# Kernel tuning notes

Hardware: AMD Instinct MI355X
Metric: run time of the kernel (lower is better)

The kernel has to match this reference:

```python
import jax, jax.numpy as jnp
import numpy as np

C = 64            # x_channel (d_model)
D = 2 * C         # d_inner (expand=2)
N = C // 2        # d_state
K = 4             # scan directions
R = -(-C // 16)   # dt_rank = ceil(d_model/16)
Bsz, H, W = 2, 48, 48
EPS = 1e-5


def setup_inputs() -> dict:
    key = jax.random.key(0)
    ks = jax.random.split(key, 8)
    g = lambda k, shp, s: jax.random.normal(k, shp, dtype=jnp.float32) * s
    return {
        "fufea1": g(ks[0], (Bsz, C, H, W), 1.0),
        "ln_g": jnp.ones((C,), jnp.float32),
        "ln_b": jnp.zeros((C,), jnp.float32),
        "in_proj_w": g(ks[1], (2 * D, C), C ** -0.5),
        "conv_w": g(ks[2], (D, 1, 3, 3), 1.0 / 3.0),   # depthwise 3x3
        "conv_b": g(ks[3], (D,), 0.02),
        "x_proj_w": g(ks[4], (K, R + 2 * N, D), D ** -0.5),
        "dt_w": g(ks[5], (K, D, R), R ** -0.5),
        "dt_b": g(ks[6], (K, D), 0.1),
        "A_logs": jnp.log(jnp.tile(jnp.arange(1, N + 1, dtype=jnp.float32), (K, D, 1))),  # S4D-real init
        "Ds": jnp.ones((K, D), jnp.float32),
        "out_ln_g": jnp.ones((D,), jnp.float32),
        "out_ln_b": jnp.zeros((D,), jnp.float32),
        "out_proj_w": g(ks[7], (C, D), D ** -0.5),
    }


def _layernorm(x, g, b):
    mu = x.mean(-1, keepdims=True)
    var = ((x - mu) ** 2).mean(-1, keepdims=True)
    return (x - mu) * jax.lax.rsqrt(var + EPS) * g + b


def reference(fufea1, ln_g, ln_b, in_proj_w, conv_w, conv_b, x_proj_w,
              dt_w, dt_b, A_logs, Ds, out_ln_g, out_ln_b, out_proj_w):
    B, Cc, Hh, Ww = fufea1.shape
    L = Hh * Ww
    # pre-LN (over channels, channels-last)
    xn = _layernorm(fufea1.transpose(0, 2, 3, 1), ln_g, ln_b)          # (B,H,W,C)
    # SS2D: in_proj -> split x,z
    xz = xn @ in_proj_w.T                                               # (B,H,W,2D)
    x, z = jnp.split(xz, 2, axis=-1)
    x = x.transpose(0, 3, 1, 2)                                         # (B,D,H,W)
    x = jax.lax.conv_general_dilated(x, conv_w, (1, 1), "SAME",
                                     feature_group_count=D,
                                     dimension_numbers=("NCHW", "OIHW", "NCHW"))
    x = jax.nn.silu(x + conv_b[None, :, None, None])
    # 4-direction sequences: row-major, col-major, and their reverses
    x_hw = x.reshape(B, D, L)
    x_wh = x.transpose(0, 1, 3, 2).reshape(B, D, L)
    xs = jnp.stack([x_hw, x_wh], axis=1)                                # (B,2,D,L)
    xs = jnp.concatenate([xs, jnp.flip(xs, axis=-1)], axis=1)           # (B,K,D,L)
    # per-direction projections of dt, B, C
    x_dbl = jnp.einsum("bkdl,kcd->bkcl", xs, x_proj_w)
    dts, Bs, Cs = jnp.split(x_dbl, [R, R + N], axis=2)                  # (B,K,R,L),(B,K,N,L),(B,K,N,L)
    dts = jnp.einsum("bkrl,kdr->bkdl", dts, dt_w)
    delta = jax.nn.softplus(dts + dt_b[None, :, :, None])               # (B,K,D,L)
    A = -jnp.exp(A_logs)                                                # (K,D,N)
    # selective scan over L; carry h: (B,K,D,N)
    u_l = xs.transpose(3, 0, 1, 2)                                      # (L,B,K,D)
    dt_l = delta.transpose(3, 0, 1, 2)
    B_l = Bs.transpose(3, 0, 1, 2)                                      # (L,B,K,N)
    C_l = Cs.transpose(3, 0, 1, 2)

    def step(h, inp):
        u_t, d_t, b_t, c_t = inp
        dA = jnp.exp(d_t[..., None] * A)                                # (B,K,D,N)
        h = dA * h + (d_t * u_t)[..., None] * b_t[:, :, None, :]
        y = jnp.einsum("bkdn,bkn->bkd", h, c_t)
        return h, y

    h0 = jnp.zeros((B, K, D, N), xs.dtype)
    _, ys = jax.lax.scan(step, h0, (u_l, dt_l, B_l, C_l))               # ys: (L,B,K,D)
    out_y = ys.transpose(1, 2, 3, 0) + Ds[None, :, :, None] * xs        # (B,K,D,L)
    # merge the 4 directions back to row-major hw order
    inv_y = jnp.flip(out_y[:, 2:4], axis=-1)                            # (B,2,D,L)
    wh = lambda t: t.reshape(B, D, Ww, Hh).transpose(0, 1, 3, 2).reshape(B, D, L)
    y = out_y[:, 0] + inv_y[:, 0] + wh(out_y[:, 1]) + wh(inv_y[:, 1])   # (B,D,L)
    y = y.transpose(0, 2, 1).reshape(B, Hh, Ww, D)
    y = _layernorm(y, out_ln_g, out_ln_b) * jax.nn.silu(z)
    out = (y @ out_proj_w.T).transpose(0, 3, 1, 2) + fufea1             # residual add
    return out
```

## Files before the change

### kernel.cpp

```cpp
#include <hip/hip_runtime.h>

#define Cc 64
#define Dd 128
#define Nn 32
#define Kk 4
#define Rr 4
#define Bb 2
#define Hh 48
#define Ww 48
#define Ll 2304
#define EPSf 1e-5f
#define LCc 144

#if __has_builtin(__builtin_amdgcn_exp2f)
#define EXP2F __builtin_amdgcn_exp2f
#else
#define EXP2F exp2f
#endif

__device__ __forceinline__ float wsum64(float v) {
  v += __shfl_xor(v, 32);
  v += __shfl_xor(v, 16);
  v += __shfl_xor(v, 8);
  v += __shfl_xor(v, 4);
  v += __shfl_xor(v, 2);
  v += __shfl_xor(v, 1);
  return v;
}

__global__ __launch_bounds__(256) void k1_ln_inproj(
    const float* __restrict__ x, const float* __restrict__ g,
    const float* __restrict__ bta, const float* __restrict__ Wp,
    float* __restrict__ xin, float* __restrict__ zb)
{
  __shared__ float xS[16][65];
  __shared__ float xnS[16][64];
  __shared__ float xaS[128][17];
  const int tid = threadIdx.x;
  const int wv = tid >> 6, lane = tid & 63;
  const int pbase = blockIdx.x * 16;
  const int b = pbase / Ll;
  const int lbase = pbase % Ll;
  {
    const int c = tid >> 2, li0 = (tid & 3) * 4;
    const float4 v4 = *(const float4*)&x[(b * Cc + c) * Ll + lbase + li0];
    xS[li0 + 0][c] = v4.x;
    xS[li0 + 1][c] = v4.y;
    xS[li0 + 2][c] = v4.z;
    xS[li0 + 3][c] = v4.w;
  }
  __syncthreads();
  const float gv = g[lane], bv = bta[lane];
  for (int pi = 0; pi < 4; ++pi) {
    const int p = wv * 4 + pi;
    const float v = xS[p][lane];
    const float mu = wsum64(v) * (1.0f / 64.0f);
    const float dv = v - mu;
    const float var = wsum64(dv * dv) * (1.0f / 64.0f);
    const float rs = rsqrtf(var + EPSf);
    xnS[p][lane] = dv * rs * gv + bv;
  }
  __syncthreads();
  float acc[4][4];
  #pragma unroll
  for (int pi = 0; pi < 4; ++pi)
    #pragma unroll
    for (int m = 0; m < 4; ++m) acc[pi][m] = 0.f;
  const float4* W4 = (const float4*)Wp;
  #pragma unroll 4
  for (int c4 = 0; c4 < 16; ++c4) {
    float4 xn4[4];
    #pragma unroll
    for (int pi = 0; pi < 4; ++pi)
      xn4[pi] = ((const float4*)xnS[wv * 4 + pi])[c4];
    #pragma unroll
    for (int m = 0; m < 4; ++m) {
      const float4 w4 = W4[(lane + 64 * m) * 16 + c4];
      #pragma unroll
      for (int pi = 0; pi < 4; ++pi)
        acc[pi][m] += xn4[pi].x * w4.x + xn4[pi].y * w4.y +
                      xn4[pi].z * w4.z + xn4[pi].w * w4.w;
    }
  }
  #pragma unroll
  for (int pi = 0; pi < 4; ++pi) {
    const int l = lbase + wv * 4 + pi;
    zb[(b * Ll + l) * Dd + lane]      = acc[pi][2];
    zb[(b * Ll + l) * Dd + lane + 64] = acc[pi][3];
    xaS[lane][wv * 4 + pi]      = acc[pi][0];
    xaS[lane + 64][wv * 4 + pi] = acc[pi][1];
  }
  __syncthreads();
  const int d = tid >> 1, off = (tid & 1) * 8;
  float* dst = &xin[(b * Dd + d) * Ll + lbase + off];
  #pragma unroll
  for (int i = 0; i < 8; ++i) dst[i] = xaS[d][off + i];
}

__global__ __launch_bounds__(512) void k3_proj(
    const float* __restrict__ xin, const float* __restrict__ cw,
    const float* __restrict__ cb, const float* __restrict__ xpw,
    const float* __restrict__ dtw, const float* __restrict__ dtb,
    float* __restrict__ xc, float2* __restrict__ dd2,
    float* __restrict__ Bm, float* __restrict__ Cm)
{
  __shared__ float xinS[128][30];
  __shared__ float xvS[8][132];
  __shared__ float dtsS[8][16];
  const int t = threadIdx.x;
  const int pb = blockIdx.x * 8;
  const int b = pb / Ll;
  const int lb = pb % Ll;
  const int h0 = lb / Ww, w0 = lb % Ww;
  for (int i = t; i < 3840; i += 512) {
    const int d = i / 30, j = i % 30;
    const int r = j / 10, c = j % 10;
    const int hh = h0 + r - 1, ww = w0 + c - 1;
    float v = 0.f;
    if (hh >= 0 && hh < Hh && ww >= 0 && ww < Ww)
      v = xin[(b * Dd + d) * Ll + hh * Ww + ww];
    xinS[d][j] = v;
  }
  __syncthreads();
  for (int i = t; i < 1024; i += 512) {
    const int pi = i >> 7, d = i & 127;
    float acc = cb[d];
    #pragma unroll
    for (int r = 0; r < 3; ++r)
      #pragma unroll
      for (int c = 0; c < 3; ++c)
        acc += xinS[d][r * 10 + pi + c] * cw[d * 9 + r * 3 + c];
    const float sig = 1.0f / (1.0f + __expf(-acc));
    xvS[pi][d] = acc * sig;
  }
  __syncthreads();
  for (int i = t; i < 1024; i += 512) {
    const int d = i >> 3, pi = i & 7;
    xc[(b * Dd + d) * Ll + lb + pi] = xvS[pi][d];
  }
  if (t < 272) {
    const int k = t / 68, c = t % 68;
    const size_t bkL = (size_t)(b * Kk + k) * Ll;
    float acc[8];
    #pragma unroll
    for (int pi = 0; pi < 8; ++pi) acc[pi] = 0.f;
    const float4* w4p = (const float4*)(xpw + (k * 68 + c) * 128);
    for (int d4 = 0; d4 < 32; ++d4) {
      const float4 w4 = w4p[d4];
      #pragma unroll
      for (int pi = 0; pi < 8; ++pi) {
        const float4 x4 = ((const float4*)xvS[pi])[d4];
        acc[pi] += x4.x * w4.x + x4.y * w4.y + x4.z * w4.z + x4.w * w4.w;
      }
    }
    #pragma unroll
    for (int pi = 0; pi < 8; ++pi) {
      const int l0 = lb + pi;
      const int h = l0 / Ww, w = l0 % Ww;
      int lk;
      if      (k == 0) lk = l0;
      else if (k == 1) lk = w * Hh + h;
      else if (k == 2) lk = Ll - 1 - l0;
      else             lk = Ll - 1 - (w * Hh + h);
      if (c < Rr)            dtsS[pi][k * 4 + c] = acc[pi];
      else if (c < Rr + Nn)  Bm[(bkL + lk) * Nn + (c - Rr)] = acc[pi];
      else                   Cm[(bkL + lk) * Nn + (c - Rr - Nn)] = acc[pi];
    }
  }
  __syncthreads();
  {
    const int k = t >> 7, dd = t & 127;
    const float4 dw = *(const float4*)&dtw[(k * Dd + dd) * 4];
    const float biasv = dtb[k * Dd + dd];
    float2* drow = dd2 + ((size_t)((b * Kk + k) * Dd) + dd) * Ll;
    float2 buf[8];
    #pragma unroll
    for (int pi = 0; pi < 8; ++pi) {
      const float a = biasv
          + dtsS[pi][k * 4 + 0] * dw.x + dtsS[pi][k * 4 + 1] * dw.y
          + dtsS[pi][k * 4 + 2] * dw.z + dtsS[pi][k * 4 + 3] * dw.w;
      const float sp = (a > 20.f) ? a : log1pf(__expf(a));
      buf[pi] = make_float2(sp, sp * xvS[pi][dd]);
    }
    if (k == 0) {
      float4* f4 = (float4*)(drow + lb);
      #pragma unroll
      for (int j = 0; j < 4; ++j)
        f4[j] = make_float4(buf[2 * j].x, buf[2 * j].y, buf[2 * j + 1].x, buf[2 * j + 1].y);
    } else if (k == 2) {
      float4* f4 = (float4*)(drow + (Ll - 8 - lb));
      #pragma unroll
      for (int j = 0; j < 4; ++j)
        f4[j] = make_float4(buf[7 - 2 * j].x, buf[7 - 2 * j].y, buf[6 - 2 * j].x, buf[6 - 2 * j].y);
    } else {
      #pragma unroll
      for (int pi = 0; pi < 8; ++pi) {
        const int l0 = lb + pi;
        const int h = l0 / Ww, w = l0 % Ww;
        int lk = w * Hh + h;
        if (k == 3) lk = Ll - 1 - lk;
        drow[lk] = buf[pi];
      }
    }
  }
}

__global__ __launch_bounds__(512) void k4_scan(
    const float2* __restrict__ dd2, const float* __restrict__ Bm,
    const float* __restrict__ Cm, const float* __restrict__ Alogs,
    float* __restrict__ ys)
{
  __shared__ float hendS[16][32];
  __shared__ float carryS[16][32];
  __shared__ float sumDS[16];
  __shared__ float pS[16][8][36];
  const int tid = threadIdx.x;
  const int s = tid >> 5, n = tid & 31;
  const int blk = blockIdx.x;
  const int bk = blk & 7;
  const int d = blk >> 3;
  const int b = bk >> 2, k = bk & 3;
  const float An = -__expf(Alogs[(k * Dd + d) * Nn + n]);
  const float AnE = An * 1.44269504f;
  const size_t bkL = (size_t)(b * Kk + k) * Ll;
  const float2* dP = dd2 + ((size_t)((b * Kk + k) * Dd) + d) * Ll;
  const float* bP = Bm + bkL * Nn + n;
  const float* cP = Cm + bkL * Nn + n;
  const int lbeg = s * LCc;
  float hA = 0.f, sumD = 0.f;
  {
    const float4* q4 = (const float4*)(dP + lbeg);
    const float* bl = bP + (size_t)lbeg * Nn;
    float4 qa = q4[0], qb = q4[1];
    float b0 = bl[0], b1 = bl[Nn], b2 = bl[2 * Nn], b3 = bl[3 * Nn];
    for (int it = 0; it < LCc / 4; ++it) {
      q4 += 2; bl += 4 * Nn;
      const float4 qa_n = q4[0], qb_n = q4[1];
      const float b0n = bl[0], b1n = bl[Nn], b2n = bl[2 * Nn], b3n = bl[3 * Nn];
      hA = EXP2F(qa.x * AnE) * hA + qa.y * b0;
      hA = EXP2F(qa.z * AnE) * hA + qa.w * b1;
      hA = EXP2F(qb.x * AnE) * hA + qb.y * b2;
      hA = EXP2F(qb.z * AnE) * hA + qb.w * b3;
      sumD += (qa.x + qa.z) + (qb.x + qb.z);
      qa = qa_n; qb = qb_n; b0 = b0n; b1 = b1n; b2 = b2n; b3 = b3n;
    }
  }
  hendS[s][n] = hA;
  if (n == 0) sumDS[s] = sumD;
  __syncthreads();
  if (tid < 32) {
    float carry = 0.f;
    #pragma unroll
    for (int s2 = 0; s2 < 16; ++s2) {
      carryS[s2][tid] = carry;
      carry = EXP2F(AnE * sumDS[s2]) * carry + hendS[s2][tid];
    }
  }
  __syncthreads();
  float h = carryS[s][n];
  float* yP = ys + ((size_t)((b * Kk + k) * Dd) + d) * Ll + lbeg;
  const float4* q4 = (const float4*)(dP + lbeg);
  const float* bl = bP + (size_t)lbeg * Nn;
  const float* cl = cP + (size_t)lbeg * Nn;
  const int rrow = n & 7, qtr = n >> 3;
  float4 qa = q4[0], qb = q4[1];
  float b0 = bl[0], b1 = bl[Nn], b2 = bl[2 * Nn], b3 = bl[3 * Nn];
  float c0 = cl[0], c1 = cl[Nn], c2 = cl[2 * Nn], c3 = cl[3 * Nn];
  for (int t8 = 0; t8 < LCc / 8; ++t8) {
    #pragma unroll
    for (int half = 0; half < 2; ++half) {
      q4 += 2; bl += 4 * Nn; cl += 4 * Nn;
      const float4 qa_n = q4[0], qb_n = q4[1];
      const float b0n = bl[0], b1n = bl[Nn], b2n = bl[2 * Nn], b3n = bl[3 * Nn];
      const float c0n = cl[0], c1n = cl[Nn], c2n = cl[2 * Nn], c3n = cl[3 * Nn];
      h = EXP2F(qa.x * AnE) * h + qa.y * b0; pS[s][half * 4 + 0][n] = h * c0;
      h = EXP2F(qa.z * AnE) * h + qa.w * b1; pS[s][half * 4 + 1][n] = h * c1;
      h = EXP2F(qb.x * AnE) * h + qb.y * b2; pS[s][half * 4 + 2][n] = h * c2;
      h = EXP2F(qb.z * AnE) * h + qb.w * b3; pS[s][half * 4 + 3][n] = h * c3;
      qa = qa_n; qb = qb_n; b0 = b0n; b1 = b1n; b2 = b2n; b3 = b3n;
      c0 = c0n; c1 = c1n; c2 = c2n; c3 = c3n;
    }
    const float4 a4 = *(const float4*)&pS[s][rrow][qtr * 8];
    const float4 d4 = *(const float4*)&pS[s][rrow][qtr * 8 + 4];
    float sum = ((a4.x + a4.y) + (a4.z + a4.w)) + ((d4.x + d4.y) + (d4.z + d4.w));
    sum += __shfl_xor(sum, 8);
    sum += __shfl_xor(sum, 16);
    if (n < 8) yP[t8 * 8 + n] = sum;
  }
}

__global__ __launch_bounds__(256) void k5_merge(
    const float* __restrict__ ys, const float* __restrict__ zb,
    const float* __restrict__ og, const float* __restrict__ ob,
    const float* __restrict__ Wo, const float* __restrict__ resid,
    const float* __restrict__ xc, const float* __restrict__ DsP,
    float* __restrict__ out)
{
  __shared__ float ysS[4][16][128];
  __shared__ float tS[16][128];
  __shared__ float oS[64][17];
  __shared__ float xcS[16][128];
  const int tid = threadIdx.x;
  const int wv = tid >> 6, lane = tid & 63;
  const int pbase = blockIdx.x * 16;
  const int b = pbase / Ll;
  const int lbase = pbase % Ll;
  const int hrow = lbase / Ww, w0 = lbase % Ww;
  {
    const int dch = tid & 127, seg = tid >> 7;
    {
      const float4 a4 = *(const float4*)&xc[(b * Dd + dch) * Ll + lbase + seg * 8];
      const float4 c4 = *(const float4*)&xc[(b * Dd + dch) * Ll + lbase + seg * 8 + 4];
      xcS[seg * 8 + 0][dch] = a4.x; xcS[seg * 8 + 1][dch] = a4.y;
      xcS[seg * 8 + 2][dch] = a4.z; xcS[seg * 8 + 3][dch] = a4.w;
      xcS[seg * 8 + 4][dch] = c4.x; xcS[seg * 8 + 5][dch] = c4.y;
      xcS[seg * 8 + 6][dch] = c4.z; xcS[seg * 8 + 7][dch] = c4.w;
    }
    {
      const size_t r0 = ((size_t)(b * Kk + 0) * Dd + dch) * Ll + lbase + seg * 8;
      const float4 a4 = *(const float4*)&ys[r0];
      const float4 c4 = *(const float4*)&ys[r0 + 4];
      ysS[0][seg * 8 + 0][dch] = a4.x; ysS[0][seg * 8 + 1][dch] = a4.y;
      ysS[0][seg * 8 + 2][dch] = a4.z; ysS[0][seg * 8 + 3][dch] = a4.w;
      ysS[0][seg * 8 + 4][dch] = c4.x; ysS[0][seg * 8 + 5][dch] = c4.y;
      ysS[0][seg * 8 + 6][dch] = c4.z; ysS[0][seg * 8 + 7][dch] = c4.w;
    }
    {
      const size_t r2 = ((size_t)(b * Kk + 2) * Dd + dch) * Ll + (Ll - 16 - lbase) + seg * 8;
      const float4 a4 = *(const float4*)&ys[r2];
      const float4 c4 = *(const float4*)&ys[r2 + 4];
      ysS[2][15 - seg * 8 - 0][dch] = a4.x; ysS[2][15 - seg * 8 - 1][dch] = a4.y;
      ysS[2][15 - seg * 8 - 2][dch] = a4.z; ysS[2][15 - seg * 8 - 3][dch] = a4.w;
      ysS[2][15 - seg * 8 - 4][dch] = c4.x; ysS[2][15 - seg * 8 - 5][dch] = c4.y;
      ysS[2][15 - seg * 8 - 6][dch] = c4.z; ysS[2][15 - seg * 8 - 7][dch] = c4.w;
    }
    {
      const size_t r1 = ((size_t)(b * Kk + 1) * Dd + dch) * Ll;
      const size_t r3 = ((size_t)(b * Kk + 3) * Dd + dch) * Ll;
      #pragma unroll
      for (int j = 0; j < 8; ++j) {
        const int p = seg * 8 + j;
        const int l1 = (w0 + p) * Hh + hrow;
        ysS[1][p][dch] = ys[r1 + l1];
        ysS[3][p][dch] = ys[r3 + (Ll - 1 - l1)];
      }
    }
  }
  float sDs[2];
  #pragma unroll
  for (int m = 0; m < 2; ++m) {
    const int dch = lane + 64 * m;
    sDs[m] = DsP[dch] + DsP[Dd + dch] + DsP[2 * Dd + dch] + DsP[3 * Dd + dch];
  }
  __syncthreads();
  for (int pi = 0; pi < 4; ++pi) {
    const int p = wv * 4 + pi;
    const int l0 = lbase + p;
    float tv[2];
    #pragma unroll
    for (int m = 0; m < 2; ++m) {
      const int dch = lane + 64 * m;
      tv[m] = ysS[0][p][dch] + ysS[1][p][dch] + ysS[2][p][dch] + ysS[3][p][dch]
            + sDs[m] * xcS[p][dch];
    }
    const float mu = wsum64(tv[0] + tv[1]) * (1.0f / 128.0f);
    const float q = wsum64((tv[0] - mu) * (tv[0] - mu) +
                           (tv[1] - mu) * (tv[1] - mu)) * (1.0f / 128.0f);
    const float rs = rsqrtf(q + EPSf);
    #pragma unroll
    for (int m = 0; m < 2; ++m) {
      const int dch = lane + 64 * m;
      const float zz = zb[(size_t)(b * Ll + l0) * Dd + dch];
      const float sig = 1.0f / (1.0f + __expf(-zz));
      tS[p][dch] = ((tv[m] - mu) * rs * og[dch] + ob[dch]) * (zz * sig);
    }
  }
  __syncthreads();
  float acc[4] = {0.f, 0.f, 0.f, 0.f};
  const float4* W4 = (const float4*)Wo;
  for (int d4 = 0; d4 < 32; ++d4) {
    const float4 w4 = W4[lane * 32 + d4];
    #pragma unroll
    for (int pi = 0; pi < 4; ++pi) {
      const float4 t4 = ((const float4*)tS[wv * 4 + pi])[d4];
      acc[pi] += t4.x * w4.x + t4.y * w4.y + t4.z * w4.z + t4.w * w4.w;
    }
  }
  #pragma unroll
  for (int pi = 0; pi < 4; ++pi) oS[lane][wv * 4 + pi] = acc[pi];
  __syncthreads();
  const int c = tid >> 2, off = (tid & 3) * 4;
  const size_t obase = (size_t)(b * Cc + c) * Ll + lbase + off;
  const float4 r4 = *(const float4*)(resid + obase);
  float4 o4;
  o4.x = oS[c][off + 0] + r4.x;
  o4.y = oS[c][off + 1] + r4.y;
  o4.z = oS[c][off + 2] + r4.z;
  o4.w = oS[c][off + 3] + r4.w;
  *(float4*)(out + obase) = o4;
}

extern "C" void kernel_launch(void* const* d_in, const int* in_sizes, int n_in,
                              void* d_out, int out_size, void* d_ws, size_t ws_size,
                              hipStream_t stream)
{
  (void)in_sizes; (void)n_in; (void)out_size; (void)ws_size;
  const float* fufea1     = (const float*)d_in[0];
  const float* ln_g       = (const float*)d_in[1];
  const float* ln_b       = (const float*)d_in[2];
  const float* in_proj_w  = (const float*)d_in[3];
  const float* conv_w     = (const float*)d_in[4];
  const float* conv_b     = (const float*)d_in[5];
  const float* x_proj_w   = (const float*)d_in[6];
  const float* dt_w       = (const float*)d_in[7];
  const float* dt_b       = (const float*)d_in[8];
  const float* A_logs     = (const float*)d_in[9];
  const float* Ds         = (const float*)d_in[10];
  const float* out_ln_g   = (const float*)d_in[11];
  const float* out_ln_b   = (const float*)d_in[12];
  const float* out_proj_w = (const float*)d_in[13];

  float* ws = (float*)d_ws;
  float2* dd2 = (float2*)ws;
  float* Bm   = ws + 4718592;
  float* Cm   = ws + 5308416;
  float* zb   = ws + 5898240;
  float* xc   = ws + 6488064;
  float* ysb  = ws + 7077888;
  float* xin  = ws + 7077888;

  k1_ln_inproj<<<288, 256, 0, stream>>>(fufea1, ln_g, ln_b, in_proj_w, xin, zb);
  k3_proj<<<576, 512, 0, stream>>>(xin, conv_w, conv_b, x_proj_w, dt_w, dt_b,
                                   xc, dd2, Bm, Cm);
  k4_scan<<<1024, 512, 0, stream>>>(dd2, Bm, Cm, A_logs, ysb);
  k5_merge<<<288, 256, 0, stream>>>(ysb, zb, out_ln_g, out_ln_b, out_proj_w, fufea1,
                                    xc, Ds, (float*)d_out);
}
```

Baseline: 218.3 us.

## Single-pass chunked scan with truncated carry correction and transposed B/C layout

The chunked selective scan now runs once, starting each chunk from a zero state and writing outputs directly, instead of a separate state pass followed by a full recompute pass. After the carry between chunks is computed, only the decaying carry contribution is added back, and that loop stops early once the decay makes it negligible according to a bound built from the carry size, the largest |C| and the slowest decay rate. B and C are also stored with time as the innermost dimension so each lane can read them as float4 vectors. This removes roughly half of the scan arithmetic and memory traffic. In exchange the result is approximate, with error controlled by a fixed threshold, and the correction adds a serial shuffle reduction per timestep.

New measurement: 378.5 us. 73.4% more time.

```diff
diff --git a/kernel.cpp b/kernel.cpp
--- a/kernel.cpp
+++ b/kernel.cpp
@@ -25,6 +25,15 @@
   v += __shfl_xor(v, 4);
   v += __shfl_xor(v, 2);
   v += __shfl_xor(v, 1);
+  return v;
+}
+
+__device__ __forceinline__ float hmax32(float v) {
+  v = fmaxf(v, __shfl_xor(v, 1));
+  v = fmaxf(v, __shfl_xor(v, 2));
+  v = fmaxf(v, __shfl_xor(v, 4));
+  v = fmaxf(v, __shfl_xor(v, 8));
+  v = fmaxf(v, __shfl_xor(v, 16));
   return v;
 }
 
@@ -140,7 +149,6 @@
   }
   if (t < 272) {
     const int k = t / 68, c = t % 68;
-    const size_t bkL = (size_t)(b * Kk + k) * Ll;
     float acc[8];
     #pragma unroll
     for (int pi = 0; pi < 8; ++pi) acc[pi] = 0.f;
@@ -162,9 +170,12 @@
       else if (k == 1) lk = w * Hh + h;
       else if (k == 2) lk = Ll - 1 - l0;
       else             lk = Ll - 1 - (w * Hh + h);
-      if (c < Rr)            dtsS[pi][k * 4 + c] = acc[pi];
-      else if (c < Rr + Nn)  Bm[(bkL + lk) * Nn + (c - Rr)] = acc[pi];
-      else                   Cm[(bkL + lk) * Nn + (c - Rr - Nn)] = acc[pi];
+      if (c < Rr)
+        dtsS[pi][k * 4 + c] = acc[pi];
+      else if (c < Rr + Nn)
+        Bm[((size_t)(b * Kk + k) * Nn + (c - Rr)) * Ll + lk] = acc[pi];
+      else
+        Cm[((size_t)(b * Kk + k) * Nn + (c - Rr - Nn)) * Ll + lk] = acc[pi];
     }
   }
   __syncthreads();
@@ -213,6 +224,7 @@
   __shared__ float hendS[16][32];
   __shared__ float carryS[16][32];
   __shared__ float sumDS[16];
+  __shared__ float cmaxS[16];
   __shared__ float pS[16][8][36];
   const int tid = threadIdx.x;
   const int s = tid >> 5, n = tid & 31;
@@ -222,31 +234,45 @@
   const int b = bk >> 2, k = bk & 3;
   const float An = -__expf(Alogs[(k * Dd + d) * Nn + n]);
   const float AnE = An * 1.44269504f;
-  const size_t bkL = (size_t)(b * Kk + k) * Ll;
   const float2* dP = dd2 + ((size_t)((b * Kk + k) * Dd) + d) * Ll;
-  const float* bP = Bm + bkL * Nn + n;
-  const float* cP = Cm + bkL * Nn + n;
+  const size_t rowBC = (size_t)(b * Kk + k) * Nn + n;
+  const float* bRow = Bm + rowBC * Ll;
+  const float* cRow = Cm + rowBC * Ll;
   const int lbeg = s * LCc;
-  float hA = 0.f, sumD = 0.f;
-  {
-    const float4* q4 = (const float4*)(dP + lbeg);
-    const float* bl = bP + (size_t)lbeg * Nn;
-    float4 qa = q4[0], qb = q4[1];
-    float b0 = bl[0], b1 = bl[Nn], b2 = bl[2 * Nn], b3 = bl[3 * Nn];
-    for (int it = 0; it < LCc / 4; ++it) {
-      q4 += 2; bl += 4 * Nn;
+  float* yP = ys + ((size_t)((b * Kk + k) * Dd) + d) * Ll + lbeg;
+
+  float h = 0.f, sumD = 0.f, cmx = 0.f;
+  const float4* q4 = (const float4*)(dP + lbeg);
+  const float4* b4 = (const float4*)(bRow + lbeg);
+  const float4* c4 = (const float4*)(cRow + lbeg);
+  const int rrow = n & 7, qtr = n >> 3;
+  float4 qa = q4[0], qb = q4[1];
+  float4 bv = b4[0], cv = c4[0];
+  for (int t8 = 0; t8 < LCc / 8; ++t8) {
+    #pragma unroll
+    for (int half = 0; half < 2; ++half) {
+      q4 += 2; b4 += 1; c4 += 1;
       const float4 qa_n = q4[0], qb_n = q4[1];
-      const float b0n = bl[0], b1n = bl[Nn], b2n = bl[2 * Nn], b3n = bl[3 * Nn];
-      hA = EXP2F(qa.x * AnE) * hA + qa.y * b0;
-      hA = EXP2F(qa.z * AnE) * hA + qa.w * b1;
-      hA = EXP2F(qb.x * AnE) * hA + qb.y * b2;
-      hA = EXP2F(qb.z * AnE) * hA + qb.w * b3;
+      const float4 bv_n = b4[0], cv_n = c4[0];
+      h = EXP2F(qa.x * AnE) * h + qa.y * bv.x; pS[s][half * 4 + 0][n] = h * cv.x;
+      h = EXP2F(qa.z * AnE) * h + qa.w * bv.y; pS[s][half * 4 + 1][n] = h * cv.y;
+      h = EXP2F(qb.x * AnE) * h + qb.y * bv.z; pS[s][half * 4 + 2][n] = h * cv.z;
+      h = EXP2F(qb.z * AnE) * h + qb.w * bv.w; pS[s][half * 4 + 3][n] = h * cv.w;
       sumD += (qa.x + qa.z) + (qb.x + qb.z);
-      qa = qa_n; qb = qb_n; b0 = b0n; b1 = b1n; b2 = b2n; b3 = b3n;
-    }
-  }
-  hendS[s][n] = hA;
-  if (n == 0) sumDS[s] = sumD;
+      cmx = fmaxf(cmx, fmaxf(fmaxf(fabsf(cv.x), fabsf(cv.y)),
+                             fmaxf(fabsf(cv.z), fabsf(cv.w))));
+      qa = qa_n; qb = qb_n; bv = bv_n; cv = cv_n;
+    }
+    const float4 a4 = *(const float4*)&pS[s][rrow][qtr * 8];
+    const float4 d4v = *(const float4*)&pS[s][rrow][qtr * 8 + 4];
+    float sum = ((a4.x + a4.y) + (a4.z + a4.w)) + ((d4v.x + d4v.y) + (d4v.z + d4v.w));
+    sum += __shfl_xor(sum, 8);
+    sum += __shfl_xor(sum, 16);
+    if (n < 8) yP[t8 * 8 + n] = sum;
+  }
+  hendS[s][n] = h;
+  const float cmxAll = hmax32(cmx);
+  if (n == 0) { sumDS[s] = sumD; cmaxS[s] = cmxAll; }
   __syncthreads();
   if (tid < 32) {
     float carry = 0.f;
@@ -257,35 +283,27 @@
     }
   }
   __syncthreads();
-  float h = carryS[s][n];
-  float* yP = ys + ((size_t)((b * Kk + k) * Dd) + d) * Ll + lbeg;
-  const float4* q4 = (const float4*)(dP + lbeg);
-  const float* bl = bP + (size_t)lbeg * Nn;
-  const float* cl = cP + (size_t)lbeg * Nn;
-  const int rrow = n & 7, qtr = n >> 3;
-  float4 qa = q4[0], qb = q4[1];
-  float b0 = bl[0], b1 = bl[Nn], b2 = bl[2 * Nn], b3 = bl[3 * Nn];
-  float c0 = cl[0], c1 = cl[Nn], c2 = cl[2 * Nn], c3 = cl[3 * Nn];
-  for (int t8 = 0; t8 < LCc / 8; ++t8) {
-    #pragma unroll
-    for (int half = 0; half < 2; ++half) {
-      q4 += 2; bl += 4 * Nn; cl += 4 * Nn;
-      const float4 qa_n = q4[0], qb_n = q4[1];
-      const float b0n = bl[0], b1n = bl[Nn], b2n = bl[2 * Nn], b3n = bl[3 * Nn];
-      const float c0n = cl[0], c1n = cl[Nn], c2n = cl[2 * Nn], c3n = cl[3 * Nn];
-      h = EXP2F(qa.x * AnE) * h + qa.y * b0; pS[s][half * 4 + 0][n] = h * c0;
-      h = EXP2F(qa.z * AnE) * h + qa.w * b1; pS[s][half * 4 + 1][n] = h * c1;
-      h = EXP2F(qb.x * AnE) * h + qb.y * b2; pS[s][half * 4 + 2][n] = h * c2;
-      h = EXP2F(qb.z * AnE) * h + qb.w * b3; pS[s][half * 4 + 3][n] = h * c3;
-      qa = qa_n; qb = qb_n; b0 = b0n; b1 = b1n; b2 = b2n; b3 = b3n;
-      c0 = c0n; c1 = c1n; c2 = c2n; c3 = c3n;
-    }
-    const float4 a4 = *(const float4*)&pS[s][rrow][qtr * 8];
-    const float4 d4 = *(const float4*)&pS[s][rrow][qtr * 8 + 4];
-    float sum = ((a4.x + a4.y) + (a4.z + a4.w)) + ((d4.x + d4.y) + (d4.z + d4.w));
-    sum += __shfl_xor(sum, 8);
-    sum += __shfl_xor(sum, 16);
-    if (n < 8) yP[t8 * 8 + n] = sum;
+  const float carry = carryS[s][n];
+  const float mc = hmax32(fabsf(carry));
+  const float AmaxE = hmax32(AnE);
+  const float Pstop = log2f(mc * cmaxS[s] * 3.2e6f) / (-AmaxE);
+  if (Pstop > 0.f) {
+    float hc = carry, P = 0.f;
+    const float2* dQ = dP + lbeg;
+    const float* cQ = cRow + lbeg;
+    for (int t = 0; t < LCc; ++t) {
+      if (P >= Pstop) break;
+      const float dlt = dQ[t].x;
+      hc *= EXP2F(dlt * AnE);
+      P += dlt;
+      float contrib = hc * cQ[t];
+      contrib += __shfl_xor(contrib, 1);
+      contrib += __shfl_xor(contrib, 2);
+      contrib += __shfl_xor(contrib, 4);
+      contrib += __shfl_xor(contrib, 8);
+      contrib += __shfl_xor(contrib, 16);
+      if (n == 0) yP[t] += contrib;
+    }
   }
 }
 
```

## Split chunked scan into local pass plus early-terminating carry correction

Applied to the files above, without the earlier changes.

The first pass of the chunked selective scan now runs from a zero state and writes each chunk's local outputs directly. The second pass no longer re-runs the full recurrence. It propagates only the incoming carry, which is decayed by the cumulative dt times A, and adds its contribution to y. That pass stops once a bound built from the running max of |C|, the max |carry| and the slowest-decaying A shows the remaining contribution is negligible. This removes most of the second read of dt, B and C, at the cost of a read-modify-write of y and a tolerance-based truncation that adds small absolute error.

Measured after the change: 202.6 us. 1.08x faster.

```diff
diff --git a/kernel.cpp b/kernel.cpp
--- a/kernel.cpp
+++ b/kernel.cpp
@@ -25,6 +25,15 @@
   v += __shfl_xor(v, 4);
   v += __shfl_xor(v, 2);
   v += __shfl_xor(v, 1);
+  return v;
+}
+
+__device__ __forceinline__ float hmax32(float v) {
+  v = fmaxf(v, __shfl_xor(v, 1));
+  v = fmaxf(v, __shfl_xor(v, 2));
+  v = fmaxf(v, __shfl_xor(v, 4));
+  v = fmaxf(v, __shfl_xor(v, 8));
+  v = fmaxf(v, __shfl_xor(v, 16));
   return v;
 }
 
@@ -213,6 +222,7 @@
   __shared__ float hendS[16][32];
   __shared__ float carryS[16][32];
   __shared__ float sumDS[16];
+  __shared__ float cmaxS[16];
   __shared__ float pS[16][8][36];
   const int tid = threadIdx.x;
   const int s = tid >> 5, n = tid & 31;
@@ -227,26 +237,45 @@
   const float* bP = Bm + bkL * Nn + n;
   const float* cP = Cm + bkL * Nn + n;
   const int lbeg = s * LCc;
-  float hA = 0.f, sumD = 0.f;
+  float* yP = ys + ((size_t)((b * Kk + k) * Dd) + d) * Ll + lbeg;
+  const int rrow = n & 7, qtr = n >> 3;
+
+  float h = 0.f, sumD = 0.f, cmx = 0.f;
   {
     const float4* q4 = (const float4*)(dP + lbeg);
     const float* bl = bP + (size_t)lbeg * Nn;
+    const float* cl = cP + (size_t)lbeg * Nn;
     float4 qa = q4[0], qb = q4[1];
     float b0 = bl[0], b1 = bl[Nn], b2 = bl[2 * Nn], b3 = bl[3 * Nn];
-    for (int it = 0; it < LCc / 4; ++it) {
-      q4 += 2; bl += 4 * Nn;
-      const float4 qa_n = q4[0], qb_n = q4[1];
-      const float b0n = bl[0], b1n = bl[Nn], b2n = bl[2 * Nn], b3n = bl[3 * Nn];
-      hA = EXP2F(qa.x * AnE) * hA + qa.y * b0;
-      hA = EXP2F(qa.z * AnE) * hA + qa.w * b1;
-      hA = EXP2F(qb.x * AnE) * hA + qb.y * b2;
-      hA = EXP2F(qb.z * AnE) * hA + qb.w * b3;
-      sumD += (qa.x + qa.z) + (qb.x + qb.z);
-      qa = qa_n; qb = qb_n; b0 = b0n; b1 = b1n; b2 = b2n; b3 = b3n;
-    }
-  }
-  hendS[s][n] = hA;
-  if (n == 0) sumDS[s] = sumD;
+    float c0 = cl[0], c1 = cl[Nn], c2 = cl[2 * Nn], c3 = cl[3 * Nn];
+    for (int t8 = 0; t8 < LCc / 8; ++t8) {
+      #pragma unroll
+      for (int half = 0; half < 2; ++half) {
+        q4 += 2; bl += 4 * Nn; cl += 4 * Nn;
+        const float4 qa_n = q4[0], qb_n = q4[1];
+        const float b0n = bl[0], b1n = bl[Nn], b2n = bl[2 * Nn], b3n = bl[3 * Nn];
+        const float c0n = cl[0], c1n = cl[Nn], c2n = cl[2 * Nn], c3n = cl[3 * Nn];
+        h = EXP2F(qa.x * AnE) * h + qa.y * b0; pS[s][half * 4 + 0][n] = h * c0;
+        h = EXP2F(qa.z * AnE) * h + qa.w * b1; pS[s][half * 4 + 1][n] = h * c1;
+        h = EXP2F(qb.x * AnE) * h + qb.y * b2; pS[s][half * 4 + 2][n] = h * c2;
+        h = EXP2F(qb.z * AnE) * h + qb.w * b3; pS[s][half * 4 + 3][n] = h * c3;
+        sumD += (qa.x + qa.z) + (qb.x + qb.z);
+        cmx = fmaxf(cmx, fmaxf(fmaxf(fabsf(c0), fabsf(c1)),
+                               fmaxf(fabsf(c2), fabsf(c3))));
+        qa = qa_n; qb = qb_n; b0 = b0n; b1 = b1n; b2 = b2n; b3 = b3n;
+        c0 = c0n; c1 = c1n; c2 = c2n; c3 = c3n;
+      }
+      const float4 a4 = *(const float4*)&pS[s][rrow][qtr * 8];
+      const float4 d4v = *(const float4*)&pS[s][rrow][qtr * 8 + 4];
+      float sum = ((a4.x + a4.y) + (a4.z + a4.w)) + ((d4v.x + d4v.y) + (d4v.z + d4v.w));
+      sum += __shfl_xor(sum, 8);
+      sum += __shfl_xor(sum, 16);
+      if (n < 8) yP[t8 * 8 + n] = sum;
+    }
+  }
+  hendS[s][n] = h;
+  const float cmxAll = hmax32(cmx);
+  if (n == 0) { sumDS[s] = sumD; cmaxS[s] = cmxAll; }
   __syncthreads();
   if (tid < 32) {
     float carry = 0.f;
@@ -257,35 +286,34 @@
     }
   }
   __syncthreads();
-  float h = carryS[s][n];
-  float* yP = ys + ((size_t)((b * Kk + k) * Dd) + d) * Ll + lbeg;
-  const float4* q4 = (const float4*)(dP + lbeg);
-  const float* bl = bP + (size_t)lbeg * Nn;
-  const float* cl = cP + (size_t)lbeg * Nn;
-  const int rrow = n & 7, qtr = n >> 3;
-  float4 qa = q4[0], qb = q4[1];
-  float b0 = bl[0], b1 = bl[Nn], b2 = bl[2 * Nn], b3 = bl[3 * Nn];
-  float c0 = cl[0], c1 = cl[Nn], c2 = cl[2 * Nn], c3 = cl[3 * Nn];
-  for (int t8 = 0; t8 < LCc / 8; ++t8) {
-    #pragma unroll
-    for (int half = 0; half < 2; ++half) {
-      q4 += 2; bl += 4 * Nn; cl += 4 * Nn;
-      const float4 qa_n = q4[0], qb_n = q4[1];
-      const float b0n = bl[0], b1n = bl[Nn], b2n = bl[2 * Nn], b3n = bl[3 * Nn];
-      const float c0n = cl[0], c1n = cl[Nn], c2n = cl[2 * Nn], c3n = cl[3 * Nn];
-      h = EXP2F(qa.x * AnE) * h + qa.y * b0; pS[s][half * 4 + 0][n] = h * c0;
-      h = EXP2F(qa.z * AnE) * h + qa.w * b1; pS[s][half * 4 + 1][n] = h * c1;
-      h = EXP2F(qb.x * AnE) * h + qb.y * b2; pS[s][half * 4 + 2][n] = h * c2;
-      h = EXP2F(qb.z * AnE) * h + qb.w * b3; pS[s][half * 4 + 3][n] = h * c3;
-      qa = qa_n; qb = qb_n; b0 = b0n; b1 = b1n; b2 = b2n; b3 = b3n;
-      c0 = c0n; c1 = c1n; c2 = c2n; c3 = c3n;
-    }
-    const float4 a4 = *(const float4*)&pS[s][rrow][qtr * 8];
-    const float4 d4 = *(const float4*)&pS[s][rrow][qtr * 8 + 4];
-    float sum = ((a4.x + a4.y) + (a4.z + a4.w)) + ((d4.x + d4.y) + (d4.z + d4.w));
-    sum += __shfl_xor(sum, 8);
-    sum += __shfl_xor(sum, 16);
-    if (n < 8) yP[t8 * 8 + n] = sum;
+  const float carry = carryS[s][n];
+  const float mc = hmax32(fabsf(carry));
+  const float AmaxE = hmax32(AnE);
+  const float Pstop = log2f(mc * cmaxS[s] * 3.2e6f) / (-AmaxE);
+  {
+    float hc = carry, P = 0.f;
+    const float4* q4 = (const float4*)(dP + lbeg);
+    const float* cl = cP + (size_t)lbeg * Nn;
+    for (int t8 = 0; t8 < LCc / 8; ++t8) {
+      if (!(P < Pstop)) break;
+      #pragma unroll
+      for (int half = 0; half < 2; ++half) {
+        const float4 qa = q4[0], qb = q4[1];
+        q4 += 2;
+        hc *= EXP2F(qa.x * AnE); pS[s][half * 4 + 0][n] = hc * cl[0];
+        hc *= EXP2F(qa.z * AnE); pS[s][half * 4 + 1][n] = hc * cl[Nn];
+        hc *= EXP2F(qb.x * AnE); pS[s][half * 4 + 2][n] = hc * cl[2 * Nn];
+        hc *= EXP2F(qb.z * AnE); pS[s][half * 4 + 3][n] = hc * cl[3 * Nn];
+        P += (qa.x + qa.z) + (qb.x + qb.z);
+        cl += 4 * Nn;
+      }
+      const float4 a4 = *(const float4*)&pS[s][rrow][qtr * 8];
+      const float4 d4v = *(const float4*)&pS[s][rrow][qtr * 8 + 4];
+      float sum = ((a4.x + a4.y) + (a4.z + a4.w)) + ((d4v.x + d4v.y) + (d4v.z + d4v.w));
+      sum += __shfl_xor(sum, 8);
+      sum += __shfl_xor(sum, 16);
+      if (n < 8) yP[t8 * 8 + n] += sum;
+    }
   }
 }
 
```
